# Performance work log

Hardware: AMD Instinct MI355X
Metric: run time of the kernel (lower is better)

Reference implementation:

```python
import jax, jax.numpy as jnp
import numpy as np

B, S, H = 1, 1024, 1024
E = 1024          # expert_dim
NEXP = 16         # num_experts
TOPK = 2
ALPHA = 1.702
LIMIT = 7.0


def setup_inputs() -> dict:
    key = jax.random.key(0)
    ks = jax.random.split(key, 8)
    hidden_states = jax.random.normal(ks[0], (B, S, H), dtype=jnp.float32)
    # router (gate): Linear(H, NEXP) with bias
    Wg = jax.random.normal(ks[1], (NEXP, H), dtype=jnp.float32) / np.sqrt(H)
    bg = jax.random.normal(ks[2], (NEXP,), dtype=jnp.float32) * 0.01
    # per-expert gate_up_proj: Linear(H, 2E) -> store as [NEXP, H, 2E]
    Wgu = jax.random.normal(ks[3], (NEXP, H, 2 * E), dtype=jnp.float32) / np.sqrt(H)
    bgu = jax.random.normal(ks[4], (NEXP, 2 * E), dtype=jnp.float32) * 0.01
    # per-expert down_proj: Linear(E, H) -> store as [NEXP, E, H]
    Wd = jax.random.normal(ks[5], (NEXP, E, H), dtype=jnp.float32) / np.sqrt(E)
    bd = jax.random.normal(ks[6], (NEXP, H), dtype=jnp.float32) * 0.01
    return {"hidden_states": hidden_states, "Wg": Wg, "bg": bg,
            "Wgu": Wgu, "bgu": bgu, "Wd": Wd, "bd": bd}


def _moe_forward(x, Wg, bg, Wgu, bgu, Wd, bd):
    b, s, h = x.shape
    xt = x.reshape(-1, h)                                   # [T, H]
    # router
    logits = xt @ Wg.T + bg                                 # [T, NEXP]
    # gpt_oss routing: topk over raw logits, softmax over selected
    top_vals, top_idx = jax.lax.top_k(logits, TOPK)         # [T, K]
    rw = jax.nn.softmax(top_vals.astype(jnp.float32), axis=-1).astype(xt.dtype)
    # combine weight per (token, expert): zero for unselected experts
    onehot = jax.nn.one_hot(top_idx, NEXP, dtype=xt.dtype)  # [T, K, NEXP]
    cw = jnp.einsum("tk,tke->te", rw, onehot)               # [T, NEXP]
    # dense expert compute (reference math identical to gather/scatter version)
    gu = jnp.einsum("th,ehf->tef", xt, Wgu) + bgu[None]     # [T, NEXP, 2E]
    gate = gu[..., ::2]
    up = gu[..., 1::2]
    gate = jnp.minimum(gate, LIMIT)
    up = jnp.clip(up, -LIMIT, LIMIT)
    glu = gate * jax.nn.sigmoid(gate * ALPHA)
    gated = (up + 1.0) * glu                                # [T, NEXP, E]
    out_e = jnp.einsum("tef,efh->teh", gated, Wd) + bd[None]  # [T, NEXP, H]
    out = jnp.einsum("teh,te->th", out_e, cw)               # [T, H]
    return out.reshape(b, s, h)


def reference(hidden_states, Wg, bg, Wgu, bgu, Wd, bd):
    return _moe_forward(hidden_states, Wg, bg, Wgu, bgu, Wd, bd)
```

## Files before the change

### kernel.cpp

```cpp
#include <hip/hip_runtime.h>
#include <hip/hip_bf16.h>

#define NT 1024
#define HD 1024
#define ED 1024
#define F2D 2048
#define NEXPERT 16
#define GROWS 2304
#define ALPHA_C 1.702f
#define LIMIT_C 7.0f

typedef float f32x4 __attribute__((ext_vector_type(4)));
typedef float fv4 __attribute__((ext_vector_type(4)));
typedef short short8 __attribute__((ext_vector_type(8)));
typedef unsigned int u32x4 __attribute__((ext_vector_type(4)));

__device__ __forceinline__ unsigned short f2bf(float x) {
  union { float f; unsigned int u; } v; v.f = x;
  unsigned int r = v.u + 0x7FFFu + ((v.u >> 16) & 1u);
  return (unsigned short)(r >> 16);
}
__device__ __forceinline__ unsigned int pk2(float lo, float hi) {
  return (unsigned int)f2bf(lo) | ((unsigned int)f2bf(hi) << 16);
}
__device__ __forceinline__ fv4 ldnt4(const float* p) {
  return __builtin_nontemporal_load((const fv4*)p);
}
__device__ __forceinline__ void async16(const void* g, void* l) {
  __builtin_amdgcn_global_load_lds((const __attribute__((address_space(1))) void*)g,
                                   (__attribute__((address_space(3))) void*)l, 16, 0, 0);
}

#define BT_TRANSPOSE_STORE(DST)                                                         \
  {                                                                                     \
    unsigned int w0p = pk2(b0[0], b1[0]);                                               \
    unsigned int w1p = pk2(b0[1], b1[1]);                                               \
    unsigned int w2p = pk2(b0[2], b1[2]);                                               \
    unsigned int w3p = pk2(b0[3], b1[3]);                                               \
    unsigned int X0 = sub == 0 ? w0p : sub == 1 ? w1p : sub == 2 ? w2p : w3p;           \
    unsigned int X1 = sub == 0 ? w1p : sub == 1 ? w0p : sub == 2 ? w3p : w2p;           \
    unsigned int X2 = sub == 0 ? w2p : sub == 1 ? w3p : sub == 2 ? w0p : w1p;           \
    unsigned int X3 = sub == 0 ? w3p : sub == 1 ? w2p : sub == 2 ? w1p : w0p;           \
    unsigned int r0 = X0;                                                               \
    unsigned int r1 = (unsigned int)__builtin_amdgcn_update_dpp((int)X1, (int)X1, 0xB1, 0xF, 0xF, 0); \
    unsigned int r2 = (unsigned int)__builtin_amdgcn_update_dpp((int)X2, (int)X2, 0x4E, 0xF, 0xF, 0); \
    unsigned int r3 = (unsigned int)__builtin_amdgcn_update_dpp((int)X3, (int)X3, 0x1B, 0xF, 0xF, 0); \
    u32x4 tt;                                                                           \
    tt[0] = sub == 0 ? r0 : sub == 1 ? r1 : sub == 2 ? r2 : r3;                         \
    tt[1] = sub == 0 ? r1 : sub == 1 ? r0 : sub == 2 ? r3 : r2;                         \
    tt[2] = sub == 0 ? r2 : sub == 1 ? r3 : sub == 2 ? r0 : r1;                         \
    tt[3] = sub == 0 ? r3 : sub == 1 ? r2 : sub == 2 ? r1 : r0;                         \
    *(u32x4*)(DST) = tt;                                                                \
  }

__global__ __launch_bounds__(256) void k_router(const float* __restrict__ x,
                                                const float* __restrict__ Wg,
                                                const float* __restrict__ bg,
                                                const float* __restrict__ bd,
                                                int* __restrict__ e01,
                                                float* __restrict__ w0f,
                                                float* __restrict__ w1f,
                                                unsigned short* __restrict__ Xbf,
                                                float* __restrict__ out) {
  const int t = blockIdx.x;
  const int tid = threadIdx.x;
  const int w = tid >> 6;
  const int l = tid & 63;
  const float4* x4 = (const float4*)(x + (size_t)t * HD);
  {
    float4 v = x4[tid];
    unsigned int* dst = (unsigned int*)(Xbf + (size_t)t * HD + tid * 4);
    dst[0] = pk2(v.x, v.y); dst[1] = pk2(v.z, v.w);
  }
  const int e = l & 15, qq = l >> 4;
  const float4* wg4 = (const float4*)(Wg + (size_t)e * HD);
  float s = 0.f;
#pragma unroll 4
  for (int j = 0; j < 16; ++j) {
    const int idx = w * 64 + qq + 4 * j;
    float4 a = x4[idx], b = wg4[idx];
    s += a.x * b.x + a.y * b.y + a.z * b.z + a.w * b.w;
  }
  s += __shfl_xor(s, 16);
  s += __shfl_xor(s, 32);
  __shared__ float slog[4][16];
  if (l < 16) slog[w][e] = s;
  __syncthreads();
  float v0 = -1e30f, v1 = -1e30f; int i0 = 0, i1 = 0;
  for (int k2 = 0; k2 < 16; ++k2) {
    float lv = slog[0][k2] + slog[1][k2] + slog[2][k2] + slog[3][k2] + bg[k2];
    if (lv > v0) { v1 = v0; i1 = i0; v0 = lv; i0 = k2; }
    else if (lv > v1) { v1 = lv; i1 = k2; }
  }
  const float w0 = 1.f / (1.f + __expf(v1 - v0));
  const float w1 = 1.f - w0;
  if (tid == 0) {
    e01[t] = i0 | (i1 << 8);
    w0f[t] = w0;
    w1f[t] = w1;
  }
  const float4* bd0 = (const float4*)(bd + (size_t)i0 * HD);
  const float4* bd1 = (const float4*)(bd + (size_t)i1 * HD);
  float4 a = bd0[tid], b = bd1[tid];
  float4 r;
  r.x = w0 * a.x + w1 * b.x;
  r.y = w0 * a.y + w1 * b.y;
  r.z = w0 * a.z + w1 * b.z;
  r.w = w0 * a.w + w1 * b.w;
  ((float4*)(out + (size_t)t * HD))[tid] = r;
}

__global__ __launch_bounds__(1024) void k_scan(const int* __restrict__ e01,
                                               const float* __restrict__ w0f,
                                               const float* __restrict__ w1f,
                                               int* __restrict__ cnt,
                                               int* __restrict__ off,
                                               int* __restrict__ gtok,
                                               float* __restrict__ gwt) {
  __shared__ int scnt[NEXPERT];
  __shared__ int soff[NEXPERT];
  __shared__ int scur[NEXPERT];
  const int t = threadIdx.x;
  if (t < NEXPERT) { scnt[t] = 0; scur[t] = 0; }
  __syncthreads();
  const int p = e01[t];
  const int e0 = p & 255, e1 = p >> 8;
  atomicAdd(&scnt[e0], 1);
  atomicAdd(&scnt[e1], 1);
  __syncthreads();
  if (t == 0) {
    int a = 0;
    for (int e = 0; e < NEXPERT; ++e) { soff[e] = a; off[e] = a; cnt[e] = scnt[e]; a += scnt[e]; }
  }
  __syncthreads();
  int s0 = atomicAdd(&scur[e0], 1);
  gtok[soff[e0] + s0] = t; gwt[soff[e0] + s0] = w0f[t];
  int s1 = atomicAdd(&scur[e1], 1);
  gtok[soff[e1] + s1] = t; gwt[soff[e1] + s1] = w1f[t];
}

#define BSTG1T 20
__global__ __launch_bounds__(512, 1) void k_gemm1(const unsigned short* __restrict__ Xbf,
                                                  const float* __restrict__ Wgu,
                                                  const float* __restrict__ bgu,
                                                  const int* __restrict__ cnt,
                                                  const int* __restrict__ off,
                                                  const int* __restrict__ gtok,
                                                  unsigned short* __restrict__ Gact) {
  const int e = blockIdx.z;
  const int Ne = cnt[e];
  const int mtile = blockIdx.y;
  if (mtile * 256 >= Ne) return;
  const int ntile = blockIdx.x;
  const int tid = threadIdx.x;
  const int lane = tid & 63;
  const int wv = tid >> 6;
  const int wm = wv >> 1;
  const int wn = wv & 1;
  const int q = lane >> 4;
  const int fr = lane & 15;
  const int base = off[e] + mtile * 256;

  __shared__ unsigned short Alds[2][256 * 32];
  __shared__ unsigned int Blds[2][128 * BSTG1T];

  const int ar0 = wv * 32 + (lane >> 2);
  const int ar1 = ar0 + 16;
  const int ags0 = base + (((mtile * 256 + ar0) < Ne) ? ar0 : 0);
  const int ags1 = base + (((mtile * 256 + ar1) < Ne) ? ar1 : 0);
  const unsigned short* agp0 = Xbf + (size_t)gtok[ags0] * HD + (lane & 3) * 8;
  const unsigned short* agp1 = Xbf + (size_t)gtok[ags1] * HD + (lane & 3) * 8;
  const int aofs = wv * 1024;

  const int sub = tid & 3;
  const int qd = tid >> 2;
  const int kblock = qd >> 5;
  const int colgrp = qd & 31;
  const float* Wb = Wgu + (size_t)e * HD * F2D + (size_t)(2 * (kblock * 4 + sub)) * F2D + ntile * 128 + colgrp * 4;
  const int bofs = (colgrp * 4 + sub) * BSTG1T + kblock * 4;

  f32x4 acc[4][4] = {};
  fv4 b0, b1;

  b0 = ldnt4(Wb);
  b1 = ldnt4(Wb + F2D);
  async16(agp0, Alds[0] + aofs);
  async16(agp1, Alds[0] + aofs + 512);
  BT_TRANSPOSE_STORE(Blds[0] + bofs)
  __syncthreads();

  for (int ks = 0; ks < 32; ++ks) {
    const int cur = ks & 1, nxt = cur ^ 1;
    const bool more = (ks + 1) < 32;
    if (more) {
      const float* bp = Wb + (size_t)(ks + 1) * 32 * F2D;
      b0 = ldnt4(bp);
      b1 = ldnt4(bp + F2D);
      async16(agp0 + (ks + 1) * 32, Alds[nxt] + aofs);
      async16(agp1 + (ks + 1) * 32, Alds[nxt] + aofs + 512);
    }
    short8 af[4], bfr[4];
#pragma unroll
    for (int mi = 0; mi < 4; ++mi)
      af[mi] = *(const short8*)(Alds[cur] + (wm * 64 + mi * 16 + fr) * 32 + q * 8);
#pragma unroll
    for (int ni = 0; ni < 4; ++ni)
      bfr[ni] = *(const short8*)(Blds[cur] + (wn * 64 + ni * 16 + fr) * BSTG1T + q * 4);
#pragma unroll
    for (int mi = 0; mi < 4; ++mi)
#pragma unroll
      for (int ni = 0; ni < 4; ++ni)
        acc[mi][ni] = __builtin_amdgcn_mfma_f32_16x16x32_bf16(af[mi], bfr[ni], acc[mi][ni], 0, 0, 0);
    if (more) BT_TRANSPOSE_STORE(Blds[nxt] + bofs)
    __syncthreads();
  }

  const float* bguE = bgu + (size_t)e * F2D + ntile * 128;
#pragma unroll
  for (int mi = 0; mi < 4; ++mi) {
#pragma unroll
    for (int ni = 0; ni < 4; ++ni) {
      const int coll = wn * 64 + ni * 16 + fr;
      const float bias = bguE[coll];
#pragma unroll
      for (int r = 0; r < 4; ++r) {
        const int srow = wm * 64 + mi * 16 + q * 4 + r;
        float v = acc[mi][ni][r] + bias;
        float pv = __shfl_xor(v, 1);
        float gate = (lane & 1) ? pv : v;
        float up   = (lane & 1) ? v : pv;
        gate = fminf(gate, LIMIT_C);
        up = fminf(fmaxf(up, -LIMIT_C), LIMIT_C);
        float glu = gate / (1.f + __expf(-ALPHA_C * gate));
        float val = (up + 1.f) * glu;
        if (!(lane & 1) && (mtile * 256 + srow) < Ne)
          Gact[(size_t)(base + srow) * ED + ((ntile * 128 + coll) >> 1)] = f2bf(val);
      }
    }
  }
}

#define BSTG2T 20
__global__ __launch_bounds__(512, 2) void k_gemm2(const unsigned short* __restrict__ Gact,
                                                  const float* __restrict__ Wd,
                                                  const int* __restrict__ cnt,
                                                  const int* __restrict__ off,
                                                  const int* __restrict__ gtok,
                                                  const float* __restrict__ gwt,
                                                  float* __restrict__ out) {
  const int e = blockIdx.z;
  const int Ne = cnt[e];
  const int mtile = blockIdx.y;
  if (mtile * 256 >= Ne) return;
  const int ntile = blockIdx.x;
  const int tid = threadIdx.x;
  const int lane = tid & 63;
  const int wv = tid >> 6;
  const int q = lane >> 4;
  const int fr = lane & 15;
  const int base = off[e] + mtile * 256;

  __shared__ unsigned int Blds[2][64 * BSTG2T];

  const unsigned short* agA0 = Gact + (size_t)(base + wv * 32 + fr) * ED + q * 8;
  const unsigned short* agA1 = agA0 + (size_t)16 * ED;

  const int sub = lane & 3;
  const float* Wb = Wd + (size_t)e * ED * HD + (size_t)(2 * (wv * 4 + sub)) * HD + ntile * 64 + (lane >> 2) * 4;
  const int bofs = lane * BSTG2T + wv * 4;

  f32x4 acc[2][4] = {};
  fv4 b0, b1;
  short8 a0, a1, a0n, a1n;

  if (tid < 256) {
    b0 = ldnt4(Wb);
    b1 = ldnt4(Wb + HD);
  }
  a0 = *(const short8*)(agA0);
  a1 = *(const short8*)(agA1);
  if (tid < 256) BT_TRANSPOSE_STORE(Blds[0] + bofs)
  __syncthreads();

  for (int ks = 0; ks < 32; ++ks) {
    const int cur = ks & 1, nxt = cur ^ 1;
    const bool more = (ks + 1) < 32;
    if (more) {
      if (tid < 256) {
        const float* bp = Wb + (size_t)(ks + 1) * 32 * HD;
        b0 = ldnt4(bp);
        b1 = ldnt4(bp + HD);
      }
      a0n = *(const short8*)(agA0 + (ks + 1) * 32);
      a1n = *(const short8*)(agA1 + (ks + 1) * 32);
    }
    short8 bfr[4];
#pragma unroll
    for (int ni = 0; ni < 4; ++ni)
      bfr[ni] = *(const short8*)(Blds[cur] + (ni * 16 + fr) * BSTG2T + q * 4);
#pragma unroll
    for (int ni = 0; ni < 4; ++ni) {
      acc[0][ni] = __builtin_amdgcn_mfma_f32_16x16x32_bf16(a0, bfr[ni], acc[0][ni], 0, 0, 0);
      acc[1][ni] = __builtin_amdgcn_mfma_f32_16x16x32_bf16(a1, bfr[ni], acc[1][ni], 0, 0, 0);
    }
    if (more && tid < 256) BT_TRANSPOSE_STORE(Blds[nxt] + bofs)
    __syncthreads();
    a0 = a0n;
    a1 = a1n;
  }

#pragma unroll
  for (int mi = 0; mi < 2; ++mi) {
#pragma unroll
    for (int r = 0; r < 4; ++r) {
      const int srow = wv * 32 + mi * 16 + q * 4 + r;
      if ((mtile * 256 + srow) < Ne) {
        const int gsl = base + srow;
        const int tok = gtok[gsl];
        const float wt = gwt[gsl];
        float* op = out + (size_t)tok * HD + ntile * 64;
#pragma unroll
        for (int ni = 0; ni < 4; ++ni) {
          const int col = ni * 16 + fr;
          atomicAdd(op + col, wt * acc[mi][ni][r]);
        }
      }
    }
  }
}

extern "C" void kernel_launch(void* const* d_in, const int* in_sizes, int n_in,
                              void* d_out, int out_size, void* d_ws, size_t ws_size,
                              hipStream_t stream) {
  const float* x   = (const float*)d_in[0];
  const float* Wg  = (const float*)d_in[1];
  const float* bg  = (const float*)d_in[2];
  const float* Wgu = (const float*)d_in[3];
  const float* bgu = (const float*)d_in[4];
  const float* Wd  = (const float*)d_in[5];
  const float* bd  = (const float*)d_in[6];
  float* out = (float*)d_out;

  int* cnt = (int*)d_ws;
  int* off = cnt + 16;
  int* e01 = off + 16;
  float* w0f = (float*)(e01 + NT);
  float* w1f = w0f + NT;
  int* gtok = (int*)(w1f + NT);
  float* gwt = (float*)(gtok + GROWS);
  unsigned short* Xbf = (unsigned short*)(gwt + GROWS);
  unsigned short* Gact = Xbf + (size_t)NT * HD;

  k_router<<<NT, 256, 0, stream>>>(x, Wg, bg, bd, e01, w0f, w1f, Xbf, out);
  k_scan<<<1, NT, 0, stream>>>(e01, w0f, w1f, cnt, off, gtok, gwt);
  k_gemm1<<<dim3(16, 2, NEXPERT), 512, 0, stream>>>(Xbf, Wgu, bgu, cnt, off, gtok, Gact);
  k_gemm2<<<dim3(16, 2, NEXPERT), 512, 0, stream>>>(Gact, Wd, cnt, off, gtok, gwt, out);
}
```

Before: 339.7 us.

## Halve GEMM N-tiles and block size to double grid parallelism

Both expert GEMM kernels change from 512-thread blocks with 128/64-column N tiles to 256-thread blocks with 64/32-column tiles, and the grid x dimension doubles to 32. Each wave now covers 64 rows and the full N tile, so the index mapping and LDS layouts are rewritten to match. The aim is more workgroups to spread across the many CUs, since only a few M-tiles per expert are active. In exchange each block loads proportionally more A (activation) data per weight column, and the LDS B row stride drops from 20 to 16, which may cause bank conflicts.

```diff
diff --git a/kernel.cpp b/kernel.cpp
--- a/kernel.cpp
+++ b/kernel.cpp
@@ -139,115 +139,13 @@
   gtok[soff[e1] + s1] = t; gwt[soff[e1] + s1] = w1f[t];
 }
 
-#define BSTG1T 20
-__global__ __launch_bounds__(512, 1) void k_gemm1(const unsigned short* __restrict__ Xbf,
-                                                  const float* __restrict__ Wgu,
-                                                  const float* __restrict__ bgu,
-                                                  const int* __restrict__ cnt,
-                                                  const int* __restrict__ off,
-                                                  const int* __restrict__ gtok,
-                                                  unsigned short* __restrict__ Gact) {
-  const int e = blockIdx.z;
-  const int Ne = cnt[e];
-  const int mtile = blockIdx.y;
-  if (mtile * 256 >= Ne) return;
-  const int ntile = blockIdx.x;
-  const int tid = threadIdx.x;
-  const int lane = tid & 63;
-  const int wv = tid >> 6;
-  const int wm = wv >> 1;
-  const int wn = wv & 1;
-  const int q = lane >> 4;
-  const int fr = lane & 15;
-  const int base = off[e] + mtile * 256;
-
-  __shared__ unsigned short Alds[2][256 * 32];
-  __shared__ unsigned int Blds[2][128 * BSTG1T];
-
-  const int ar0 = wv * 32 + (lane >> 2);
-  const int ar1 = ar0 + 16;
-  const int ags0 = base + (((mtile * 256 + ar0) < Ne) ? ar0 : 0);
-  const int ags1 = base + (((mtile * 256 + ar1) < Ne) ? ar1 : 0);
-  const unsigned short* agp0 = Xbf + (size_t)gtok[ags0] * HD + (lane & 3) * 8;
-  const unsigned short* agp1 = Xbf + (size_t)gtok[ags1] * HD + (lane & 3) * 8;
-  const int aofs = wv * 1024;
-
-  const int sub = tid & 3;
-  const int qd = tid >> 2;
-  const int kblock = qd >> 5;
-  const int colgrp = qd & 31;
-  const float* Wb = Wgu + (size_t)e * HD * F2D + (size_t)(2 * (kblock * 4 + sub)) * F2D + ntile * 128 + colgrp * 4;
-  const int bofs = (colgrp * 4 + sub) * BSTG1T + kblock * 4;
-
-  f32x4 acc[4][4] = {};
-  fv4 b0, b1;
-
-  b0 = ldnt4(Wb);
-  b1 = ldnt4(Wb + F2D);
-  async16(agp0, Alds[0] + aofs);
-  async16(agp1, Alds[0] + aofs + 512);
-  BT_TRANSPOSE_STORE(Blds[0] + bofs)
-  __syncthreads();
-
-  for (int ks = 0; ks < 32; ++ks) {
-    const int cur = ks & 1, nxt = cur ^ 1;
-    const bool more = (ks + 1) < 32;
-    if (more) {
-      const float* bp = Wb + (size_t)(ks + 1) * 32 * F2D;
-      b0 = ldnt4(bp);
-      b1 = ldnt4(bp + F2D);
-      async16(agp0 + (ks + 1) * 32, Alds[nxt] + aofs);
-      async16(agp1 + (ks + 1) * 32, Alds[nxt] + aofs + 512);
-    }
-    short8 af[4], bfr[4];
-#pragma unroll
-    for (int mi = 0; mi < 4; ++mi)
-      af[mi] = *(const short8*)(Alds[cur] + (wm * 64 + mi * 16 + fr) * 32 + q * 8);
-#pragma unroll
-    for (int ni = 0; ni < 4; ++ni)
-      bfr[ni] = *(const short8*)(Blds[cur] + (wn * 64 + ni * 16 + fr) * BSTG1T + q * 4);
-#pragma unroll
-    for (int mi = 0; mi < 4; ++mi)
-#pragma unroll
-      for (int ni = 0; ni < 4; ++ni)
-        acc[mi][ni] = __builtin_amdgcn_mfma_f32_16x16x32_bf16(af[mi], bfr[ni], acc[mi][ni], 0, 0, 0);
-    if (more) BT_TRANSPOSE_STORE(Blds[nxt] + bofs)
-    __syncthreads();
-  }
-
-  const float* bguE = bgu + (size_t)e * F2D + ntile * 128;
-#pragma unroll
-  for (int mi = 0; mi < 4; ++mi) {
-#pragma unroll
-    for (int ni = 0; ni < 4; ++ni) {
-      const int coll = wn * 64 + ni * 16 + fr;
-      const float bias = bguE[coll];
-#pragma unroll
-      for (int r = 0; r < 4; ++r) {
-        const int srow = wm * 64 + mi * 16 + q * 4 + r;
-        float v = acc[mi][ni][r] + bias;
-        float pv = __shfl_xor(v, 1);
-        float gate = (lane & 1) ? pv : v;
-        float up   = (lane & 1) ? v : pv;
-        gate = fminf(gate, LIMIT_C);
-        up = fminf(fmaxf(up, -LIMIT_C), LIMIT_C);
-        float glu = gate / (1.f + __expf(-ALPHA_C * gate));
-        float val = (up + 1.f) * glu;
-        if (!(lane & 1) && (mtile * 256 + srow) < Ne)
-          Gact[(size_t)(base + srow) * ED + ((ntile * 128 + coll) >> 1)] = f2bf(val);
-      }
-    }
-  }
-}
-
-#define BSTG2T 20
-__global__ __launch_bounds__(512, 2) void k_gemm2(const unsigned short* __restrict__ Gact,
-                                                  const float* __restrict__ Wd,
-                                                  const int* __restrict__ cnt,
-                                                  const int* __restrict__ off,
-                                                  const int* __restrict__ gtok,
-                                                  const float* __restrict__ gwt,
-                                                  float* __restrict__ out) {
+__global__ __launch_bounds__(256) void k_gemm1(const unsigned short* __restrict__ Xbf,
+                                               const float* __restrict__ Wgu,
+                                               const float* __restrict__ bgu,
+                                               const int* __restrict__ cnt,
+                                               const int* __restrict__ off,
+                                               const int* __restrict__ gtok,
+                                               unsigned short* __restrict__ Gact) {
   const int e = blockIdx.z;
   const int Ne = cnt[e];
   const int mtile = blockIdx.y;
@@ -260,67 +158,179 @@
   const int fr = lane & 15;
   const int base = off[e] + mtile * 256;
 
-  __shared__ unsigned int Blds[2][64 * BSTG2T];
-
-  const unsigned short* agA0 = Gact + (size_t)(base + wv * 32 + fr) * ED + q * 8;
-  const unsigned short* agA1 = agA0 + (size_t)16 * ED;
-
-  const int sub = lane & 3;
-  const float* Wb = Wd + (size_t)e * ED * HD + (size_t)(2 * (wv * 4 + sub)) * HD + ntile * 64 + (lane >> 2) * 4;
-  const int bofs = lane * BSTG2T + wv * 4;
-
-  f32x4 acc[2][4] = {};
+  __shared__ unsigned short Alds[2][256 * 32];
+  __shared__ unsigned int Blds[2][64 * 16];
+
+  const int arow = tid >> 2;
+  const unsigned short* agp[4];
+#pragma unroll
+  for (int j = 0; j < 4; ++j) {
+    const int r = arow + j * 64;
+    const int ags = base + (((mtile * 256 + r) < Ne) ? r : 0);
+    agp[j] = Xbf + (size_t)gtok[ags] * HD + (tid & 3) * 8;
+  }
+  const int aofs = tid * 8;
+
+  const int sub = tid & 3;
+  const int quad = tid >> 2;
+  const int colgrp = quad & 15;
+  const int kblock = quad >> 4;
+  const float* Wb = Wgu + (size_t)e * HD * F2D + (size_t)(2 * (kblock * 4 + sub)) * F2D + ntile * 64 + colgrp * 4;
+  const int bofs = (colgrp * 4 + sub) * 16 + kblock * 4;
+
+  f32x4 acc[4][4] = {};
   fv4 b0, b1;
-  short8 a0, a1, a0n, a1n;
-
-  if (tid < 256) {
-    b0 = ldnt4(Wb);
-    b1 = ldnt4(Wb + HD);
-  }
-  a0 = *(const short8*)(agA0);
-  a1 = *(const short8*)(agA1);
-  if (tid < 256) BT_TRANSPOSE_STORE(Blds[0] + bofs)
+
+  b0 = ldnt4(Wb);
+  b1 = ldnt4(Wb + F2D);
+#pragma unroll
+  for (int j = 0; j < 4; ++j)
+    async16(agp[j], Alds[0] + aofs + j * 2048);
+  BT_TRANSPOSE_STORE(Blds[0] + bofs)
   __syncthreads();
 
   for (int ks = 0; ks < 32; ++ks) {
     const int cur = ks & 1, nxt = cur ^ 1;
     const bool more = (ks + 1) < 32;
     if (more) {
-      if (tid < 256) {
+      const float* bp = Wb + (size_t)(ks + 1) * 32 * F2D;
+      b0 = ldnt4(bp);
+      b1 = ldnt4(bp + F2D);
+#pragma unroll
+      for (int j = 0; j < 4; ++j)
+        async16(agp[j] + (ks + 1) * 32, Alds[nxt] + aofs + j * 2048);
+    }
+    short8 af[4], bfr[4];
+#pragma unroll
+    for (int mi = 0; mi < 4; ++mi)
+      af[mi] = *(const short8*)(Alds[cur] + (wv * 64 + mi * 16 + fr) * 32 + q * 8);
+#pragma unroll
+    for (int ni = 0; ni < 4; ++ni)
+      bfr[ni] = *(const short8*)(Blds[cur] + (ni * 16 + fr) * 16 + q * 4);
+#pragma unroll
+    for (int mi = 0; mi < 4; ++mi)
+#pragma unroll
+      for (int ni = 0; ni < 4; ++ni)
+        acc[mi][ni] = __builtin_amdgcn_mfma_f32_16x16x32_bf16(af[mi], bfr[ni], acc[mi][ni], 0, 0, 0);
+    if (more) BT_TRANSPOSE_STORE(Blds[nxt] + bofs)
+    __syncthreads();
+  }
+
+  const float* bguE = bgu + (size_t)e * F2D + ntile * 64;
+#pragma unroll
+  for (int mi = 0; mi < 4; ++mi) {
+#pragma unroll
+    for (int ni = 0; ni < 4; ++ni) {
+      const int coll = ni * 16 + fr;
+      const float bias = bguE[coll];
+#pragma unroll
+      for (int r = 0; r < 4; ++r) {
+        const int srow = wv * 64 + mi * 16 + q * 4 + r;
+        float v = acc[mi][ni][r] + bias;
+        float pv = __shfl_xor(v, 1);
+        float gate = (lane & 1) ? pv : v;
+        float up   = (lane & 1) ? v : pv;
+        gate = fminf(gate, LIMIT_C);
+        up = fminf(fmaxf(up, -LIMIT_C), LIMIT_C);
+        float glu = gate / (1.f + __expf(-ALPHA_C * gate));
+        float val = (up + 1.f) * glu;
+        if (!(lane & 1) && (mtile * 256 + srow) < Ne)
+          Gact[(size_t)(base + srow) * ED + ((ntile * 64 + coll) >> 1)] = f2bf(val);
+      }
+    }
+  }
+}
+
+__global__ __launch_bounds__(256) void k_gemm2(const unsigned short* __restrict__ Gact,
+                                               const float* __restrict__ Wd,
+                                               const int* __restrict__ cnt,
+                                               const int* __restrict__ off,
+                                               const int* __restrict__ gtok,
+                                               const float* __restrict__ gwt,
+                                               float* __restrict__ out) {
+  const int e = blockIdx.z;
+  const int Ne = cnt[e];
+  const int mtile = blockIdx.y;
+  if (mtile * 256 >= Ne) return;
+  const int ntile = blockIdx.x;
+  const int tid = threadIdx.x;
+  const int lane = tid & 63;
+  const int wv = tid >> 6;
+  const int q = lane >> 4;
+  const int fr = lane & 15;
+  const int base = off[e] + mtile * 256;
+
+  __shared__ unsigned int Blds[2][32 * 16];
+
+  const unsigned short* agA[4];
+#pragma unroll
+  for (int mi = 0; mi < 4; ++mi)
+    agA[mi] = Gact + (size_t)(base + wv * 64 + mi * 16 + fr) * ED + q * 8;
+
+  const int sub = tid & 3;
+  const int quad = tid >> 2;
+  const int colgrp = quad & 7;
+  const int kblock = quad >> 3;
+  const float* Wb = Wd + (size_t)e * ED * HD + (size_t)(2 * (kblock * 4 + sub)) * HD + ntile * 32 + colgrp * 4;
+  const int bofs = (colgrp * 4 + sub) * 16 + kblock * 4;
+
+  f32x4 acc[4][2] = {};
+  fv4 b0, b1;
+  short8 a0, a1, a2, a3, a0n, a1n, a2n, a3n;
+
+  if (tid < 128) {
+    b0 = ldnt4(Wb);
+    b1 = ldnt4(Wb + HD);
+  }
+  a0 = *(const short8*)(agA[0]);
+  a1 = *(const short8*)(agA[1]);
+  a2 = *(const short8*)(agA[2]);
+  a3 = *(const short8*)(agA[3]);
+  if (tid < 128) BT_TRANSPOSE_STORE(Blds[0] + bofs)
+  __syncthreads();
+
+  for (int ks = 0; ks < 32; ++ks) {
+    const int cur = ks & 1, nxt = cur ^ 1;
+    const bool more = (ks + 1) < 32;
+    if (more) {
+      if (tid < 128) {
         const float* bp = Wb + (size_t)(ks + 1) * 32 * HD;
         b0 = ldnt4(bp);
         b1 = ldnt4(bp + HD);
       }
-      a0n = *(const short8*)(agA0 + (ks + 1) * 32);
-      a1n = *(const short8*)(agA1 + (ks + 1) * 32);
-    }
-    short8 bfr[4];
-#pragma unroll
-    for (int ni = 0; ni < 4; ++ni)
-      bfr[ni] = *(const short8*)(Blds[cur] + (ni * 16 + fr) * BSTG2T + q * 4);
-#pragma unroll
-    for (int ni = 0; ni < 4; ++ni) {
+      a0n = *(const short8*)(agA[0] + (ks + 1) * 32);
+      a1n = *(const short8*)(agA[1] + (ks + 1) * 32);
+      a2n = *(const short8*)(agA[2] + (ks + 1) * 32);
+      a3n = *(const short8*)(agA[3] + (ks + 1) * 32);
+    }
+    short8 bfr[2];
+#pragma unroll
+    for (int ni = 0; ni < 2; ++ni)
+      bfr[ni] = *(const short8*)(Blds[cur] + (ni * 16 + fr) * 16 + q * 4);
+#pragma unroll
+    for (int ni = 0; ni < 2; ++ni) {
       acc[0][ni] = __builtin_amdgcn_mfma_f32_16x16x32_bf16(a0, bfr[ni], acc[0][ni], 0, 0, 0);
       acc[1][ni] = __builtin_amdgcn_mfma_f32_16x16x32_bf16(a1, bfr[ni], acc[1][ni], 0, 0, 0);
-    }
-    if (more && tid < 256) BT_TRANSPOSE_STORE(Blds[nxt] + bofs)
+      acc[2][ni] = __builtin_amdgcn_mfma_f32_16x16x32_bf16(a2, bfr[ni], acc[2][ni], 0, 0, 0);
+      acc[3][ni] = __builtin_amdgcn_mfma_f32_16x16x32_bf16(a3, bfr[ni], acc[3][ni], 0, 0, 0);
+    }
+    if (more && tid < 128) BT_TRANSPOSE_STORE(Blds[nxt] + bofs)
     __syncthreads();
-    a0 = a0n;
-    a1 = a1n;
-  }
-
-#pragma unroll
-  for (int mi = 0; mi < 2; ++mi) {
+    a0 = a0n; a1 = a1n; a2 = a2n; a3 = a3n;
+  }
+
+#pragma unroll
+  for (int mi = 0; mi < 4; ++mi) {
 #pragma unroll
     for (int r = 0; r < 4; ++r) {
-      const int srow = wv * 32 + mi * 16 + q * 4 + r;
+      const int srow = wv * 64 + mi * 16 + q * 4 + r;
       if ((mtile * 256 + srow) < Ne) {
         const int gsl = base + srow;
         const int tok = gtok[gsl];
         const float wt = gwt[gsl];
-        float* op = out + (size_t)tok * HD + ntile * 64;
-#pragma unroll
-        for (int ni = 0; ni < 4; ++ni) {
+        float* op = out + (size_t)tok * HD + ntile * 32;
+#pragma unroll
+        for (int ni = 0; ni < 2; ++ni) {
           const int col = ni * 16 + fr;
           atomicAdd(op + col, wt * acc[mi][ni][r]);
         }
@@ -353,6 +363,6 @@
 
   k_router<<<NT, 256, 0, stream>>>(x, Wg, bg, bd, e01, w0f, w1f, Xbf, out);
   k_scan<<<1, NT, 0, stream>>>(e01, w0f, w1f, cnt, off, gtok, gwt);
-  k_gemm1<<<dim3(16, 2, NEXPERT), 512, 0, stream>>>(Xbf, Wgu, bgu, cnt, off, gtok, Gact);
-  k_gemm2<<<dim3(16, 2, NEXPERT), 512, 0, stream>>>(Gact, Wd, cnt, off, gtok, gwt, out);
-}
+  k_gemm1<<<dim3(32, 2, NEXPERT), 256, 0, stream>>>(Xbf, Wgu, bgu, cnt, off, gtok, Gact);
+  k_gemm2<<<dim3(32, 2, NEXPERT), 256, 0, stream>>>(Gact, Wd, cnt, off, gtok, gwt, out);
+}
```

Result: slower. 376.4 us (+10.8%).

## Retile gemm1 to 256-thread 64-col tiles with swizzled LDS, stage gemm2 A through LDS

Applied to the files above, without the earlier changes.

gemm1 moves from 512-thread blocks covering 128 output columns to 256-thread blocks covering 64 columns, doubling the grid along N. Each wave now owns 64 rows across the full tile. The B tile is unpadded and XOR-swizzled in LDS, and the A tile load and read use a matching swizzle, to avoid bank conflicts. gemm2 now loads its A operand through an async LDS double buffer instead of direct global register loads. The goal is more blocks in flight for gemm1 and better-overlapped A fetch in gemm2, at the cost of more total B-weight traffic per row tile and extra LDS in gemm2.

```diff
diff --git a/kernel.cpp b/kernel.cpp
--- a/kernel.cpp
+++ b/kernel.cpp
@@ -139,14 +139,13 @@
   gtok[soff[e1] + s1] = t; gwt[soff[e1] + s1] = w1f[t];
 }
 
-#define BSTG1T 20
-__global__ __launch_bounds__(512, 1) void k_gemm1(const unsigned short* __restrict__ Xbf,
-                                                  const float* __restrict__ Wgu,
-                                                  const float* __restrict__ bgu,
-                                                  const int* __restrict__ cnt,
-                                                  const int* __restrict__ off,
-                                                  const int* __restrict__ gtok,
-                                                  unsigned short* __restrict__ Gact) {
+__global__ __launch_bounds__(256) void k_gemm1(const unsigned short* __restrict__ Xbf,
+                                               const float* __restrict__ Wgu,
+                                               const float* __restrict__ bgu,
+                                               const int* __restrict__ cnt,
+                                               const int* __restrict__ off,
+                                               const int* __restrict__ gtok,
+                                               unsigned short* __restrict__ Gact) {
   const int e = blockIdx.z;
   const int Ne = cnt[e];
   const int mtile = blockIdx.y;
@@ -155,37 +154,41 @@
   const int tid = threadIdx.x;
   const int lane = tid & 63;
   const int wv = tid >> 6;
-  const int wm = wv >> 1;
-  const int wn = wv & 1;
   const int q = lane >> 4;
   const int fr = lane & 15;
+  const int xq = q ^ ((fr >> 1) & 3);
   const int base = off[e] + mtile * 256;
 
   __shared__ unsigned short Alds[2][256 * 32];
-  __shared__ unsigned int Blds[2][128 * BSTG1T];
-
-  const int ar0 = wv * 32 + (lane >> 2);
-  const int ar1 = ar0 + 16;
-  const int ags0 = base + (((mtile * 256 + ar0) < Ne) ? ar0 : 0);
-  const int ags1 = base + (((mtile * 256 + ar1) < Ne) ? ar1 : 0);
-  const unsigned short* agp0 = Xbf + (size_t)gtok[ags0] * HD + (lane & 3) * 8;
-  const unsigned short* agp1 = Xbf + (size_t)gtok[ags1] * HD + (lane & 3) * 8;
-  const int aofs = wv * 1024;
+  __shared__ unsigned int Blds[2][64 * 16];
+
+  const int arow = tid >> 2;
+  const int cs = (tid & 3) ^ ((arow >> 1) & 3);
+  const unsigned short* agp[4];
+#pragma unroll
+  for (int j = 0; j < 4; ++j) {
+    const int r = arow + j * 64;
+    const int ags = base + (((mtile * 256 + r) < Ne) ? r : 0);
+    agp[j] = Xbf + (size_t)gtok[ags] * HD + cs * 8;
+  }
+  const int aofs = tid * 8;
 
   const int sub = tid & 3;
-  const int qd = tid >> 2;
-  const int kblock = qd >> 5;
-  const int colgrp = qd & 31;
-  const float* Wb = Wgu + (size_t)e * HD * F2D + (size_t)(2 * (kblock * 4 + sub)) * F2D + ntile * 128 + colgrp * 4;
-  const int bofs = (colgrp * 4 + sub) * BSTG1T + kblock * 4;
+  const int quad = tid >> 2;
+  const int colgrp = quad & 15;
+  const int kblock = quad >> 4;
+  const float* Wb = Wgu + (size_t)e * HD * F2D + (size_t)(2 * (kblock * 4 + sub)) * F2D + ntile * 64 + colgrp * 4;
+  const int bcol = colgrp * 4 + sub;
+  const int bofs = bcol * 16 + (kblock ^ ((bcol >> 1) & 3)) * 4;
 
   f32x4 acc[4][4] = {};
   fv4 b0, b1;
 
   b0 = ldnt4(Wb);
   b1 = ldnt4(Wb + F2D);
-  async16(agp0, Alds[0] + aofs);
-  async16(agp1, Alds[0] + aofs + 512);
+#pragma unroll
+  for (int j = 0; j < 4; ++j)
+    async16(agp[j], Alds[0] + aofs + j * 2048);
   BT_TRANSPOSE_STORE(Blds[0] + bofs)
   __syncthreads();
 
@@ -196,16 +199,17 @@
       const float* bp = Wb + (size_t)(ks + 1) * 32 * F2D;
       b0 = ldnt4(bp);
       b1 = ldnt4(bp + F2D);
-      async16(agp0 + (ks + 1) * 32, Alds[nxt] + aofs);
-      async16(agp1 + (ks + 1) * 32, Alds[nxt] + aofs + 512);
+#pragma unroll
+      for (int j = 0; j < 4; ++j)
+        async16(agp[j] + (ks + 1) * 32, Alds[nxt] + aofs + j * 2048);
     }
     short8 af[4], bfr[4];
 #pragma unroll
     for (int mi = 0; mi < 4; ++mi)
-      af[mi] = *(const short8*)(Alds[cur] + (wm * 64 + mi * 16 + fr) * 32 + q * 8);
+      af[mi] = *(const short8*)(Alds[cur] + (wv * 64 + mi * 16 + fr) * 32 + xq * 8);
 #pragma unroll
     for (int ni = 0; ni < 4; ++ni)
-      bfr[ni] = *(const short8*)(Blds[cur] + (wn * 64 + ni * 16 + fr) * BSTG1T + q * 4);
+      bfr[ni] = *(const short8*)(Blds[cur] + (ni * 16 + fr) * 16 + xq * 4);
 #pragma unroll
     for (int mi = 0; mi < 4; ++mi)
 #pragma unroll
@@ -215,16 +219,16 @@
     __syncthreads();
   }
 
-  const float* bguE = bgu + (size_t)e * F2D + ntile * 128;
+  const float* bguE = bgu + (size_t)e * F2D + ntile * 64;
 #pragma unroll
   for (int mi = 0; mi < 4; ++mi) {
 #pragma unroll
     for (int ni = 0; ni < 4; ++ni) {
-      const int coll = wn * 64 + ni * 16 + fr;
+      const int coll = ni * 16 + fr;
       const float bias = bguE[coll];
 #pragma unroll
       for (int r = 0; r < 4; ++r) {
-        const int srow = wm * 64 + mi * 16 + q * 4 + r;
+        const int srow = wv * 64 + mi * 16 + q * 4 + r;
         float v = acc[mi][ni][r] + bias;
         float pv = __shfl_xor(v, 1);
         float gate = (lane & 1) ? pv : v;
@@ -234,7 +238,7 @@
         float glu = gate / (1.f + __expf(-ALPHA_C * gate));
         float val = (up + 1.f) * glu;
         if (!(lane & 1) && (mtile * 256 + srow) < Ne)
-          Gact[(size_t)(base + srow) * ED + ((ntile * 128 + coll) >> 1)] = f2bf(val);
+          Gact[(size_t)(base + srow) * ED + ((ntile * 64 + coll) >> 1)] = f2bf(val);
       }
     }
   }
@@ -260,10 +264,13 @@
   const int fr = lane & 15;
   const int base = off[e] + mtile * 256;
 
+  __shared__ unsigned short Alds[2][256 * 32];
   __shared__ unsigned int Blds[2][64 * BSTG2T];
 
-  const unsigned short* agA0 = Gact + (size_t)(base + wv * 32 + fr) * ED + q * 8;
-  const unsigned short* agA1 = agA0 + (size_t)16 * ED;
+  const int ar0 = wv * 32 + (lane >> 2);
+  const unsigned short* agp0 = Gact + (size_t)(base + ar0) * ED + (lane & 3) * 8;
+  const unsigned short* agp1 = agp0 + (size_t)16 * ED;
+  const int aofs = wv * 1024;
 
   const int sub = lane & 3;
   const float* Wb = Wd + (size_t)e * ED * HD + (size_t)(2 * (wv * 4 + sub)) * HD + ntile * 64 + (lane >> 2) * 4;
@@ -271,14 +278,13 @@
 
   f32x4 acc[2][4] = {};
   fv4 b0, b1;
-  short8 a0, a1, a0n, a1n;
 
   if (tid < 256) {
     b0 = ldnt4(Wb);
     b1 = ldnt4(Wb + HD);
   }
-  a0 = *(const short8*)(agA0);
-  a1 = *(const short8*)(agA1);
+  async16(agp0, Alds[0] + aofs);
+  async16(agp1, Alds[0] + aofs + 512);
   if (tid < 256) BT_TRANSPOSE_STORE(Blds[0] + bofs)
   __syncthreads();
 
@@ -291,22 +297,23 @@
         b0 = ldnt4(bp);
         b1 = ldnt4(bp + HD);
       }
-      a0n = *(const short8*)(agA0 + (ks + 1) * 32);
-      a1n = *(const short8*)(agA1 + (ks + 1) * 32);
+      async16(agp0 + (ks + 1) * 32, Alds[nxt] + aofs);
+      async16(agp1 + (ks + 1) * 32, Alds[nxt] + aofs + 512);
     }
-    short8 bfr[4];
+    short8 af[2], bfr[4];
+#pragma unroll
+    for (int mi = 0; mi < 2; ++mi)
+      af[mi] = *(const short8*)(Alds[cur] + (wv * 32 + mi * 16 + fr) * 32 + q * 8);
 #pragma unroll
     for (int ni = 0; ni < 4; ++ni)
       bfr[ni] = *(const short8*)(Blds[cur] + (ni * 16 + fr) * BSTG2T + q * 4);
 #pragma unroll
-    for (int ni = 0; ni < 4; ++ni) {
-      acc[0][ni] = __builtin_amdgcn_mfma_f32_16x16x32_bf16(a0, bfr[ni], acc[0][ni], 0, 0, 0);
-      acc[1][ni] = __builtin_amdgcn_mfma_f32_16x16x32_bf16(a1, bfr[ni], acc[1][ni], 0, 0, 0);
-    }
+    for (int mi = 0; mi < 2; ++mi)
+#pragma unroll
+      for (int ni = 0; ni < 4; ++ni)
+        acc[mi][ni] = __builtin_amdgcn_mfma_f32_16x16x32_bf16(af[mi], bfr[ni], acc[mi][ni], 0, 0, 0);
     if (more && tid < 256) BT_TRANSPOSE_STORE(Blds[nxt] + bofs)
     __syncthreads();
-    a0 = a0n;
-    a1 = a1n;
   }
 
 #pragma unroll
@@ -353,6 +360,6 @@
 
   k_router<<<NT, 256, 0, stream>>>(x, Wg, bg, bd, e01, w0f, w1f, Xbf, out);
   k_scan<<<1, NT, 0, stream>>>(e01, w0f, w1f, cnt, off, gtok, gwt);
-  k_gemm1<<<dim3(16, 2, NEXPERT), 512, 0, stream>>>(Xbf, Wgu, bgu, cnt, off, gtok, Gact);
+  k_gemm1<<<dim3(32, 2, NEXPERT), 256, 0, stream>>>(Xbf, Wgu, bgu, cnt, off, gtok, Gact);
   k_gemm2<<<dim3(16, 2, NEXPERT), 512, 0, stream>>>(Gact, Wd, cnt, off, gtok, gwt, out);
 }
```

New measurement: 339.1 us. Within noise of the previous version (-0.2%).
